# Kernel optimization log

Measured on AMD Instinct MI355X. Metric: run time of the kernel, lower is better.

Reference implementation:

```python
import jax, jax.numpy as jnp
import numpy as np

N = 100000      # nodes
E = 1600000     # edges
NINP = 64       # input node features
NE = 8          # edge attr channels (spectral supports)
NOUT = 24       # nout1 == nout2
NIN = 2 * NOUT  # 48, hidden width after concat
G = 256         # graphs in batch
EPS = 1e-5


def setup_inputs() -> dict:
    key = jax.random.key(0)
    ks = jax.random.split(key, 40)
    def nrm(i, shape, s=1.0):
        return jax.random.normal(ks[i], shape, dtype=jnp.float32) * s
    inp = {}
    inp["x"] = nrm(0, (N, NINP))
    inp["edge_index"] = jax.random.randint(ks[1], (2, E), 0, N)
    inp["edge_attr"] = nrm(2, (E, NE))
    inp["batch"] = jnp.sort(jax.random.randint(ks[3], (N,), 0, G))
    i = 4
    for l, din in ((1, NINP), (2, NIN), (3, NIN)):
        inp[f"W{l}"] = nrm(i, (NE, din, NOUT), 0.1); i += 1   # SpectConv weight [K,in,out]
        inp[f"b{l}"] = jnp.zeros((NOUT,), jnp.float32)         # SpectConv bias
        inp[f"A{l}"] = nrm(i, (din, NOUT), 0.1); i += 1        # fc11 weight
        inp[f"a{l}"] = jnp.zeros((NOUT,), jnp.float32)
        inp[f"B{l}"] = nrm(i, (din, NOUT), 0.1); i += 1        # fc12 weight
        inp[f"c{l}"] = jnp.zeros((NOUT,), jnp.float32)
        inp[f"g{l}"] = jnp.ones((NIN,), jnp.float32)           # BN gamma
        inp[f"be{l}"] = jnp.zeros((NIN,), jnp.float32)         # BN beta
    inp["F1"] = nrm(i, (NIN, 32), 0.1); i += 1
    inp["f1"] = jnp.zeros((32,), jnp.float32)
    inp["F2"] = nrm(i, (32, 1), 0.1); i += 1
    inp["f2"] = jnp.zeros((1,), jnp.float32)
    return inp


def _ml3(x, src, dst, ea, W, b, A, a, Bm, c):
    # SpectConv (selfconn=False): sum_k segment_sum(ea[:,k]*x[src] -> dst) @ W[k] + b
    xs = x[src]                                    # [E, F] gather
    acc = jnp.zeros((x.shape[0], W.shape[2]), x.dtype)
    for k in range(W.shape[0]):                    # small fixed K=NE loop
        h = jax.ops.segment_sum(ea[:, k:k+1] * xs, dst, num_segments=x.shape[0])
        acc = acc + h @ W[k]
    conv = jax.nn.relu(acc + b)
    gate = jax.nn.relu(x @ A + a) * jnp.tanh(x @ Bm + c)
    return jnp.concatenate([conv, gate], axis=1)   # [N, NIN]


def _bn(x, g, b):
    # BatchNorm1d, training mode (biased batch statistics)
    m = x.mean(0)
    v = x.var(0)
    return (x - m) * jax.lax.rsqrt(v + EPS) * g + b


def reference(x, edge_index, edge_attr, batch,
              W1, b1, A1, a1, B1, c1, g1, be1,
              W2, b2, A2, a2, B2, c2, g2, be2,
              W3, b3, A3, a3, B3, c3, g3, be3,
              F1, f1, F2, f2):
    src, dst = edge_index[0], edge_index[1]
    h = _bn(_ml3(x, src, dst, edge_attr, W1, b1, A1, a1, B1, c1), g1, be1)
    h = _bn(_ml3(h, src, dst, edge_attr, W2, b2, A2, a2, B2, c2), g2, be2)
    h = _bn(_ml3(h, src, dst, edge_attr, W3, b3, A3, a3, B3, c3), g3, be3)
    sums = jax.ops.segment_sum(h, batch, num_segments=G)
    cnts = jax.ops.segment_sum(jnp.ones((h.shape[0], 1), h.dtype), batch, num_segments=G)
    pooled = sums / jnp.maximum(cnts, 1.0)         # global_mean_pool
    return jax.nn.relu(pooled @ F1 + f1) @ F2 + f2  # [G, 1]
```

## Files before the change

### kernel.cpp

```cpp
#include <hip/hip_runtime.h>
#include <hip/hip_fp16.h>
#include <math.h>

#define N_NODES 100000
#define N_EDGES 1600000
#define NGRAPH  256
#define YCOLS   240
#define EPS     1e-5f
#define BNCHUNK 100

typedef _Float16 h2v __attribute__((ext_vector_type(2)));

#if defined(__has_builtin)
#if __has_builtin(__builtin_amdgcn_fdot2)
#define HAVE_FDOT2 1
#endif
#endif

__device__ inline float dot8(float4 yraw, float4 eraw, float acc) {
#ifdef HAVE_FDOT2
  union U { float4 f; h2v v[4]; } y, e;
  y.f = yraw; e.f = eraw;
  acc = __builtin_amdgcn_fdot2(y.v[0], e.v[0], acc, false);
  acc = __builtin_amdgcn_fdot2(y.v[1], e.v[1], acc, false);
  acc = __builtin_amdgcn_fdot2(y.v[2], e.v[2], acc, false);
  acc = __builtin_amdgcn_fdot2(y.v[3], e.v[3], acc, false);
#else
  const __half2* yh = reinterpret_cast<const __half2*>(&yraw);
  const __half2* eh = reinterpret_cast<const __half2*>(&eraw);
#pragma unroll
  for (int i = 0; i < 4; i++) {
    float2 a = __half22float2(yh[i]), b = __half22float2(eh[i]);
    acc += a.x * b.x + a.y * b.y;
  }
#endif
  return acc;
}

__global__ void k_count(const int* __restrict__ dst, int* __restrict__ deg) {
  int e = blockIdx.x * blockDim.x + threadIdx.x;
  if (e < N_EDGES) atomicAdd(&deg[dst[e]], 1);
}

__global__ void k_scan1(const int* __restrict__ deg, int* __restrict__ part,
                        int* __restrict__ bsum) {
  __shared__ int lds[256];
  int t = threadIdx.x;
  int base = blockIdx.x * 1024 + t * 4;
  int v[4]; int s = 0;
#pragma unroll
  for (int i = 0; i < 4; i++) { int idx = base + i; v[i] = (idx < N_NODES) ? deg[idx] : 0; s += v[i]; }
  lds[t] = s; __syncthreads();
  for (int off = 1; off < 256; off <<= 1) {
    int x = (t >= off) ? lds[t - off] : 0;
    __syncthreads();
    lds[t] += x;
    __syncthreads();
  }
  int excl = lds[t] - s;
#pragma unroll
  for (int i = 0; i < 4; i++) { int idx = base + i; if (idx < N_NODES) part[idx] = excl; excl += v[i]; }
  if (t == 255) bsum[blockIdx.x] = lds[255];
}

__global__ void k_scan2(int* __restrict__ bsum, int nb) {
  __shared__ int lds[128];
  int t = threadIdx.x;
  int v = (t < nb) ? bsum[t] : 0;
  lds[t] = v; __syncthreads();
  for (int off = 1; off < 128; off <<= 1) {
    int x = (t >= off) ? lds[t - off] : 0;
    __syncthreads();
    lds[t] += x;
    __syncthreads();
  }
  if (t < nb) bsum[t] = lds[t] - v;
}

__global__ void k_scan3(int* __restrict__ rowptr, const int* __restrict__ bsum,
                        int* __restrict__ cursor) {
  int i = blockIdx.x * blockDim.x + threadIdx.x;
  if (i < N_NODES) {
    int v = rowptr[i] + bsum[i >> 10];
    rowptr[i] = v; cursor[i] = v;
  }
  if (i == 0) rowptr[N_NODES] = N_EDGES;
}

__global__ void k_fill(const int* __restrict__ src, const int* __restrict__ dst,
                       const float* __restrict__ ea, int* __restrict__ cursor,
                       int* __restrict__ esrc, __half* __restrict__ ea_csr) {
  int e = blockIdx.x * blockDim.x + threadIdx.x;
  if (e < N_EDGES) {
    int d = dst[e];
    int pos = atomicAdd(&cursor[d], 1);
    esrc[pos] = src[e];
    float4 a = *reinterpret_cast<const float4*>(ea + (size_t)e * 8);
    float4 b = *reinterpret_cast<const float4*>(ea + (size_t)e * 8 + 4);
    union { __half h[8]; float4 f; } u;
    u.h[0] = __float2half(a.x); u.h[1] = __float2half(a.y);
    u.h[2] = __float2half(a.z); u.h[3] = __float2half(a.w);
    u.h[4] = __float2half(b.x); u.h[5] = __float2half(b.y);
    u.h[6] = __float2half(b.z); u.h[7] = __float2half(b.w);
    *reinterpret_cast<float4*>(ea_csr + (size_t)pos * 8) = u.f;
  }
}

__global__ void k_ghist(const int* __restrict__ batch, int* __restrict__ gcnt) {
  __shared__ int lh[NGRAPH];
  int t = threadIdx.x;
  lh[t] = 0; __syncthreads();
  for (int i = blockIdx.x * 256 + t; i < N_NODES; i += gridDim.x * 256)
    atomicAdd(&lh[batch[i]], 1);
  __syncthreads();
  if (lh[t]) atomicAdd(&gcnt[t], lh[t]);
}

__global__ void k_gscan(const int* __restrict__ gcnt, int* __restrict__ gstart) {
  __shared__ int lds[NGRAPH];
  int t = threadIdx.x;
  int v = gcnt[t]; lds[t] = v; __syncthreads();
  for (int off = 1; off < NGRAPH; off <<= 1) {
    int x = (t >= off) ? lds[t - off] : 0;
    __syncthreads();
    lds[t] += x;
    __syncthreads();
  }
  gstart[t] = lds[t] - v;
  if (t == NGRAPH - 1) gstart[NGRAPH] = lds[NGRAPH - 1];
}

__global__ void k_wcat(const float* __restrict__ W, const float* __restrict__ A,
                       const float* __restrict__ B, float* __restrict__ out, int din) {
  int i = blockIdx.x * blockDim.x + threadIdx.x;
  int total = din * YCOLS;
  if (i >= total) return;
  int f = i / YCOLS, j = i - f * YCOLS;
  float v;
  if (j < 192)      { int k = j / 24, o = j - k * 24; v = W[(k * din + f) * 24 + o]; }
  else if (j < 216) v = A[f * 24 + (j - 192)];
  else              v = B[f * 24 + (j - 216)];
  out[i] = v;
}

template <int F>
__global__ __launch_bounds__(256) void k_mm(const float* __restrict__ X,
                                            const float* __restrict__ Wc,
                                            const float* __restrict__ ss,
                                            __half* __restrict__ Yh,
                                            float* __restrict__ G) {
  __shared__ float sx[16 * F];
  int t = threadIdx.x;
  int r0 = blockIdx.x * 16;
  for (int i = t; i < 16 * F; i += 256) {
    int r = i / F, f = i - r * F;
    int row = r0 + r;
    float v = (row < N_NODES) ? X[(size_t)row * F + f] : 0.f;
    if (ss) v = v * ss[f] + ss[48 + f];
    sx[i] = v;
  }
  __syncthreads();
  if (t < YCOLS) {
    float acc[16];
#pragma unroll
    for (int r = 0; r < 16; r++) acc[r] = 0.f;
    for (int f = 0; f < F; f += 4) {
      float w0 = Wc[(f + 0) * YCOLS + t];
      float w1 = Wc[(f + 1) * YCOLS + t];
      float w2 = Wc[(f + 2) * YCOLS + t];
      float w3 = Wc[(f + 3) * YCOLS + t];
#pragma unroll
      for (int r = 0; r < 16; r++) {
        const float4 xv = *reinterpret_cast<const float4*>(&sx[r * F + f]);
        acc[r] += xv.x * w0 + xv.y * w1 + xv.z * w2 + xv.w * w3;
      }
    }
    int ycol = (t % 24) * 8 + t / 24;
    int gc   = (t < 216) ? (t - 192) : (24 + t - 216);
#pragma unroll
    for (int r = 0; r < 16; r++) {
      int row = r0 + r;
      if (row < N_NODES) {
        if (t < 192) Yh[(size_t)row * 192 + ycol] = __float2half(acc[r]);
        else         G[(size_t)row * 48 + gc] = acc[r];
      }
    }
  }
}

__global__ __launch_bounds__(192) void k_agg(
    const __half* __restrict__ Yh, const float* __restrict__ G,
    const int* __restrict__ rowptr, const int* __restrict__ esrc,
    const __half* __restrict__ ea_csr,
    const float* __restrict__ bconv, const float* __restrict__ ba,
    const float* __restrict__ bc,
    float* __restrict__ h, float* __restrict__ partial) {
  __shared__ float ssum[48], ssq[48];
  __shared__ float lacc[2][4][24];
  int t = threadIdx.x;
  if (t < 48) { ssum[t] = 0.f; ssq[t] = 0.f; }
  int ln   = t / 96;
  int slot = (t / 24) % 4;
  int o    = t % 24;
  int n = blockIdx.x * 2 + ln;
  float acc = 0.f;
  if (n < N_NODES) {
    int r0 = rowptr[n], r1 = rowptr[n + 1];
    int idx = r0 + slot;
    for (; idx + 4 < r1; idx += 8) {
      int s0 = esrc[idx], s1 = esrc[idx + 4];
      float4 e0 = *reinterpret_cast<const float4*>(ea_csr + (size_t)idx * 8);
      float4 e1 = *reinterpret_cast<const float4*>(ea_csr + (size_t)(idx + 4) * 8);
      float4 y0 = *reinterpret_cast<const float4*>(Yh + (size_t)s0 * 192 + o * 8);
      float4 y1 = *reinterpret_cast<const float4*>(Yh + (size_t)s1 * 192 + o * 8);
      acc = dot8(y0, e0, acc);
      acc = dot8(y1, e1, acc);
    }
    if (idx < r1) {
      int s0 = esrc[idx];
      float4 e0 = *reinterpret_cast<const float4*>(ea_csr + (size_t)idx * 8);
      float4 y0 = *reinterpret_cast<const float4*>(Yh + (size_t)s0 * 192 + o * 8);
      acc = dot8(y0, e0, acc);
    }
  }
  lacc[ln][slot][o] = acc;
  __syncthreads();
  if (t < 48) {
    int ln2 = t / 24, oo = t % 24;
    int n2 = blockIdx.x * 2 + ln2;
    if (n2 < N_NODES) {
      float a = lacc[ln2][0][oo] + lacc[ln2][1][oo] + lacc[ln2][2][oo] + lacc[ln2][3][oo];
      float conv = fmaxf(a + bconv[oo], 0.f);
      const float* gr = &G[(size_t)n2 * 48];
      float gate = fmaxf(gr[oo] + ba[oo], 0.f) * tanhf(gr[24 + oo] + bc[oo]);
      float* hr = &h[(size_t)n2 * 48];
      hr[oo] = conv;
      hr[24 + oo] = gate;
      atomicAdd(&ssum[oo], conv);        atomicAdd(&ssq[oo], conv * conv);
      atomicAdd(&ssum[24 + oo], gate);   atomicAdd(&ssq[24 + oo], gate * gate);
    }
  }
  __syncthreads();
  if (t < 96) partial[(size_t)blockIdx.x * 96 + t] = (t < 48) ? ssum[t] : ssq[t - 48];
}

__global__ __launch_bounds__(192) void k_bnred1(const float* __restrict__ partial,
                                                int nrows,
                                                float* __restrict__ out) {
  __shared__ float lds[192];
  int t = threadIdx.x;
  int rp = t / 96;
  int c  = t % 96;
  int r0 = blockIdx.x * BNCHUNK;
  int r1 = r0 + BNCHUNK; if (r1 > nrows) r1 = nrows;
  float s = 0.f;
  for (int r = r0 + rp; r < r1; r += 2) s += partial[(size_t)r * 96 + c];
  lds[t] = s; __syncthreads();
  if (t < 96) out[(size_t)blockIdx.x * 96 + t] = lds[t] + lds[t + 96];
}

__global__ void k_bnstats(const float* __restrict__ partial, int nblk,
                          const float* __restrict__ g, const float* __restrict__ be,
                          float* __restrict__ ss) {
  __shared__ float ls[256], lq[256];
  int c = blockIdx.x, t = threadIdx.x;
  float s = 0.f, q = 0.f;
  for (int i = t; i < nblk; i += 256) { s += partial[(size_t)i * 96 + c]; q += partial[(size_t)i * 96 + 48 + c]; }
  ls[t] = s; lq[t] = q; __syncthreads();
  for (int off = 128; off > 0; off >>= 1) {
    if (t < off) { ls[t] += ls[t + off]; lq[t] += lq[t + off]; }
    __syncthreads();
  }
  if (t == 0) {
    float mean = ls[0] / (float)N_NODES;
    float var = lq[0] / (float)N_NODES - mean * mean;
    var = fmaxf(var, 0.f);
    float sc = g[c] * rsqrtf(var + EPS);
    ss[c] = sc;
    ss[48 + c] = be[c] - mean * sc;
  }
}

__global__ __launch_bounds__(240) void k_pool2(const float* __restrict__ h,
                                               const int* __restrict__ gstart,
                                               const float* __restrict__ ss,
                                               float* __restrict__ pooled) {
  __shared__ float acc[240];
  int g = blockIdx.x, t = threadIdx.x;
  int o = t % 48, r = t / 48;
  int n0 = gstart[g], n1 = gstart[g + 1];
  float s = 0.f;
  for (int n = n0 + r; n < n1; n += 5) s += h[(size_t)n * 48 + o];
  acc[t] = s; __syncthreads();
  if (t < 48) {
    float tot = acc[t] + acc[t + 48] + acc[t + 96] + acc[t + 144] + acc[t + 192];
    float cnt = (float)(n1 - n0);
    float mean = tot / fmaxf(cnt, 1.f);
    pooled[g * 48 + t] = mean * ss[t] + ss[48 + t];
  }
}

__global__ __launch_bounds__(64) void k_mlp(const float* __restrict__ pooled,
                                            const float* __restrict__ F1,
                                            const float* __restrict__ f1,
                                            const float* __restrict__ F2,
                                            const float* __restrict__ f2,
                                            float* __restrict__ out) {
  __shared__ float p[48];
  int g = blockIdx.x, t = threadIdx.x;
  if (t < 48) p[t] = pooled[g * 48 + t];
  __syncthreads();
  float r = 0.f;
  if (t < 32) {
    float s = f1[t];
#pragma unroll
    for (int c = 0; c < 48; c++) s += p[c] * F1[c * 32 + t];
    r = fmaxf(s, 0.f) * F2[t];
  }
  for (int off = 32; off > 0; off >>= 1) r += __shfl_down(r, off, 64);
  if (t == 0) out[g] = r + f2[0];
}

extern "C" void kernel_launch(void* const* d_in, const int* in_sizes, int n_in,
                              void* d_out, int out_size, void* d_ws, size_t ws_size,
                              hipStream_t stream) {
  const float* x          = (const float*)d_in[0];
  const int*   edge_index = (const int*)d_in[1];
  const float* ea         = (const float*)d_in[2];
  const int*   batch      = (const int*)d_in[3];
  const float *W[3], *bcv[3], *A[3], *ba[3], *B[3], *bc[3], *g[3], *be[3];
  for (int l = 0; l < 3; l++) {
    int base = 4 + l * 8;
    W[l]   = (const float*)d_in[base + 0];
    bcv[l] = (const float*)d_in[base + 1];
    A[l]   = (const float*)d_in[base + 2];
    ba[l]  = (const float*)d_in[base + 3];
    B[l]   = (const float*)d_in[base + 4];
    bc[l]  = (const float*)d_in[base + 5];
    g[l]   = (const float*)d_in[base + 6];
    be[l]  = (const float*)d_in[base + 7];
  }
  const float* F1 = (const float*)d_in[28];
  const float* f1 = (const float*)d_in[29];
  const float* F2 = (const float*)d_in[30];
  const float* f2 = (const float*)d_in[31];
  const int* src = edge_index;
  const int* dst = edge_index + N_EDGES;

  char* w = (char*)d_ws;
  auto alloc = [&](size_t bytes) -> char* {
    char* p = w;
    w += (bytes + 255) & ~(size_t)255;
    return p;
  };
  int nagg = (N_NODES + 1) / 2;
  int nred = (nagg + BNCHUNK - 1) / BNCHUNK;

  int*    rowptr  = (int*)alloc((N_NODES + 1) * 4);
  int*    cursor  = (int*)alloc((size_t)N_NODES * 4);
  int*    deg     = (int*)alloc((size_t)N_NODES * 4);
  int*    bsum    = (int*)alloc(128 * 4);
  int*    esrc    = (int*)alloc((size_t)N_EDGES * 4);
  __half* ea_csr  = (__half*)alloc((size_t)N_EDGES * 8 * 2);
  int*    gcnt    = (int*)alloc(NGRAPH * 4);
  int*    gstart  = (int*)alloc((NGRAPH + 1) * 4);
  float*  Wc1     = (float*)alloc(64 * 240 * 4);
  float*  Wc2     = (float*)alloc(48 * 240 * 4);
  float*  Wc3     = (float*)alloc(48 * 240 * 4);
  __half* Yh      = (__half*)alloc((size_t)N_NODES * 192 * 2);
  float*  G       = (float*)alloc((size_t)N_NODES * 48 * 4);
  float*  h       = (float*)alloc((size_t)N_NODES * 48 * 4);
  float*  partial = (float*)alloc((size_t)nagg * 96 * 4);
  float*  partial2= (float*)alloc((size_t)nred * 96 * 4);
  float*  ss1     = (float*)alloc(96 * 4);
  float*  ss2     = (float*)alloc(96 * 4);
  float*  ss3     = (float*)alloc(96 * 4);
  float*  pooled  = (float*)alloc(NGRAPH * 48 * 4);

  hipMemsetAsync(deg, 0, (size_t)N_NODES * 4, stream);
  hipMemsetAsync(gcnt, 0, NGRAPH * 4, stream);

  k_count<<<(N_EDGES + 255) / 256, 256, 0, stream>>>(dst, deg);
  int nchunk = (N_NODES + 1023) / 1024;
  k_scan1<<<nchunk, 256, 0, stream>>>(deg, rowptr, bsum);
  k_scan2<<<1, 128, 0, stream>>>(bsum, nchunk);
  k_scan3<<<(N_NODES + 255) / 256, 256, 0, stream>>>(rowptr, bsum, cursor);
  k_fill<<<(N_EDGES + 255) / 256, 256, 0, stream>>>(src, dst, ea, cursor, esrc, ea_csr);

  k_ghist<<<64, 256, 0, stream>>>(batch, gcnt);
  k_gscan<<<1, NGRAPH, 0, stream>>>(gcnt, gstart);

  k_wcat<<<(64 * YCOLS + 255) / 256, 256, 0, stream>>>(W[0], A[0], B[0], Wc1, 64);
  k_wcat<<<(48 * YCOLS + 255) / 256, 256, 0, stream>>>(W[1], A[1], B[1], Wc2, 48);
  k_wcat<<<(48 * YCOLS + 255) / 256, 256, 0, stream>>>(W[2], A[2], B[2], Wc3, 48);

  int nmm  = (N_NODES + 15) / 16;

  k_mm<64><<<nmm, 256, 0, stream>>>(x, Wc1, nullptr, Yh, G);
  k_agg<<<nagg, 192, 0, stream>>>(Yh, G, rowptr, esrc, ea_csr, bcv[0], ba[0], bc[0], h, partial);
  k_bnred1<<<nred, 192, 0, stream>>>(partial, nagg, partial2);
  k_bnstats<<<48, 256, 0, stream>>>(partial2, nred, g[0], be[0], ss1);
  k_mm<48><<<nmm, 256, 0, stream>>>(h, Wc2, ss1, Yh, G);
  k_agg<<<nagg, 192, 0, stream>>>(Yh, G, rowptr, esrc, ea_csr, bcv[1], ba[1], bc[1], h, partial);
  k_bnred1<<<nred, 192, 0, stream>>>(partial, nagg, partial2);
  k_bnstats<<<48, 256, 0, stream>>>(partial2, nred, g[1], be[1], ss2);
  k_mm<48><<<nmm, 256, 0, stream>>>(h, Wc3, ss2, Yh, G);
  k_agg<<<nagg, 192, 0, stream>>>(Yh, G, rowptr, esrc, ea_csr, bcv[2], ba[2], bc[2], h, partial);
  k_bnred1<<<nred, 192, 0, stream>>>(partial, nagg, partial2);
  k_bnstats<<<48, 256, 0, stream>>>(partial2, nred, g[2], be[2], ss3);

  k_pool2<<<NGRAPH, 240, 0, stream>>>(h, gstart, ss3, pooled);
  k_mlp<<<NGRAPH, 64, 0, stream>>>(pooled, F1, f1, F2, f2, (float*)d_out);
}
```

Before: 762.4 us.

## Use fp16 MFMA for node projection GEMM with transposed half weights

Replaces the scalar-FMA per-layer node GEMM (X times concatenated weights, 240 columns) with MFMA 16x16x32 f16 instructions. Input rows are converted to fp16 in LDS, 64 rows per block, and K is padded to 64 with zeros for the 48-wide layers. The weights are prepacked as transposed fp16. This cuts ALU work in the GEMM but adds fp16 rounding of activations and weights, and the output stores are scattered per MFMA lane.

```diff
diff --git a/kernel.cpp b/kernel.cpp
--- a/kernel.cpp
+++ b/kernel.cpp
@@ -9,7 +9,9 @@
 #define EPS     1e-5f
 #define BNCHUNK 100
 
-typedef _Float16 h2v __attribute__((ext_vector_type(2)));
+typedef _Float16 h2v  __attribute__((ext_vector_type(2)));
+typedef _Float16 f16x8 __attribute__((ext_vector_type(8)));
+typedef float    f32x4 __attribute__((ext_vector_type(4)));
 
 #if defined(__has_builtin)
 #if __has_builtin(__builtin_amdgcn_fdot2)
@@ -130,59 +132,82 @@
   if (t == NGRAPH - 1) gstart[NGRAPH] = lds[NGRAPH - 1];
 }
 
-__global__ void k_wcat(const float* __restrict__ W, const float* __restrict__ A,
-                       const float* __restrict__ B, float* __restrict__ out, int din) {
+__global__ void k_wcat_h(const float* __restrict__ W, const float* __restrict__ A,
+                         const float* __restrict__ B, __half* __restrict__ out,
+                         int din) {
   int i = blockIdx.x * blockDim.x + threadIdx.x;
-  int total = din * YCOLS;
-  if (i >= total) return;
-  int f = i / YCOLS, j = i - f * YCOLS;
-  float v;
-  if (j < 192)      { int k = j / 24, o = j - k * 24; v = W[(k * din + f) * 24 + o]; }
-  else if (j < 216) v = A[f * 24 + (j - 192)];
-  else              v = B[f * 24 + (j - 216)];
-  out[i] = v;
+  if (i >= YCOLS * 64) return;
+  int j = i / 64, f = i % 64;
+  float v = 0.f;
+  if (f < din) {
+    if (j < 192)      { int k8 = j / 24, o = j - k8 * 24; v = W[(k8 * din + f) * 24 + o]; }
+    else if (j < 216) v = A[f * 24 + (j - 192)];
+    else              v = B[f * 24 + (j - 216)];
+  }
+  out[i] = __float2half(v);
 }
 
 template <int F>
 __global__ __launch_bounds__(256) void k_mm(const float* __restrict__ X,
-                                            const float* __restrict__ Wc,
+                                            const __half* __restrict__ Wct,
                                             const float* __restrict__ ss,
                                             __half* __restrict__ Yh,
                                             float* __restrict__ G) {
-  __shared__ float sx[16 * F];
-  int t = threadIdx.x;
-  int r0 = blockIdx.x * 16;
-  for (int i = t; i < 16 * F; i += 256) {
-    int r = i / F, f = i - r * F;
-    int row = r0 + r;
-    float v = (row < N_NODES) ? X[(size_t)row * F + f] : 0.f;
-    if (ss) v = v * ss[f] + ss[48 + f];
-    sx[i] = v;
+  __shared__ _Float16 sx[64][64];
+  int t = threadIdx.x;
+  int r0 = blockIdx.x * 64;
+  constexpr int F4 = F / 4;
+  for (int i = t; i < 64 * F4; i += 256) {
+    int row = i / F4, c4 = i - row * F4;
+    int grow = r0 + row;
+    float4 v = make_float4(0.f, 0.f, 0.f, 0.f);
+    if (grow < N_NODES) {
+      v = *reinterpret_cast<const float4*>(X + (size_t)grow * F + c4 * 4);
+      if (ss) {
+        int f = c4 * 4;
+        v.x = v.x * ss[f + 0] + ss[48 + f + 0];
+        v.y = v.y * ss[f + 1] + ss[48 + f + 1];
+        v.z = v.z * ss[f + 2] + ss[48 + f + 2];
+        v.w = v.w * ss[f + 3] + ss[48 + f + 3];
+      }
+    }
+    int c = c4 * 4;
+    sx[row][c + 0] = (_Float16)v.x;
+    sx[row][c + 1] = (_Float16)v.y;
+    sx[row][c + 2] = (_Float16)v.z;
+    sx[row][c + 3] = (_Float16)v.w;
+  }
+  if (F == 48) {
+    for (int i = t; i < 64 * 16; i += 256) {
+      int row = i / 16, k = 48 + (i - (i / 16) * 16);
+      sx[row][k] = (_Float16)0.f;
+    }
   }
   __syncthreads();
-  if (t < YCOLS) {
-    float acc[16];
-#pragma unroll
-    for (int r = 0; r < 16; r++) acc[r] = 0.f;
-    for (int f = 0; f < F; f += 4) {
-      float w0 = Wc[(f + 0) * YCOLS + t];
-      float w1 = Wc[(f + 1) * YCOLS + t];
-      float w2 = Wc[(f + 2) * YCOLS + t];
-      float w3 = Wc[(f + 3) * YCOLS + t];
-#pragma unroll
-      for (int r = 0; r < 16; r++) {
-        const float4 xv = *reinterpret_cast<const float4*>(&sx[r * F + f]);
-        acc[r] += xv.x * w0 + xv.y * w1 + xv.z * w2 + xv.w * w3;
-      }
-    }
-    int ycol = (t % 24) * 8 + t / 24;
-    int gc   = (t < 216) ? (t - 192) : (24 + t - 216);
-#pragma unroll
-    for (int r = 0; r < 16; r++) {
-      int row = r0 + r;
-      if (row < N_NODES) {
-        if (t < 192) Yh[(size_t)row * 192 + ycol] = __float2half(acc[r]);
-        else         G[(size_t)row * 48 + gc] = acc[r];
+
+  int w = t >> 6, l = t & 63;
+  int lrow = l & 15;
+  int lk = (l >> 4) * 8;
+  const f16x8 a0 = *reinterpret_cast<const f16x8*>(&sx[w * 16 + lrow][lk]);
+  const f16x8 a1 = *reinterpret_cast<const f16x8*>(&sx[w * 16 + lrow][lk + 32]);
+  const _Float16* wct = reinterpret_cast<const _Float16*>(Wct);
+
+#pragma unroll
+  for (int ct = 0; ct < 15; ct++) {
+    int col = ct * 16 + lrow;
+    f16x8 b0 = *reinterpret_cast<const f16x8*>(wct + col * 64 + lk);
+    f16x8 b1 = *reinterpret_cast<const f16x8*>(wct + col * 64 + lk + 32);
+    f32x4 acc = {0.f, 0.f, 0.f, 0.f};
+    acc = __builtin_amdgcn_mfma_f32_16x16x32_f16(a0, b0, acc, 0, 0, 0);
+    acc = __builtin_amdgcn_mfma_f32_16x16x32_f16(a1, b1, acc, 0, 0, 0);
+    int ycol = (col % 24) * 8 + col / 24;
+    int gc   = (col < 216) ? (col - 192) : (24 + col - 216);
+#pragma unroll
+    for (int r = 0; r < 4; r++) {
+      int grow = r0 + w * 16 + (l >> 4) * 4 + r;
+      if (grow < N_NODES) {
+        if (col < 192) Yh[(size_t)grow * 192 + ycol] = __float2half(acc[r]);
+        else           G[(size_t)grow * 48 + gc] = acc[r];
       }
     }
   }
@@ -364,9 +389,9 @@
   __half* ea_csr  = (__half*)alloc((size_t)N_EDGES * 8 * 2);
   int*    gcnt    = (int*)alloc(NGRAPH * 4);
   int*    gstart  = (int*)alloc((NGRAPH + 1) * 4);
-  float*  Wc1     = (float*)alloc(64 * 240 * 4);
-  float*  Wc2     = (float*)alloc(48 * 240 * 4);
-  float*  Wc3     = (float*)alloc(48 * 240 * 4);
+  __half* Wct1    = (__half*)alloc((size_t)YCOLS * 64 * 2);
+  __half* Wct2    = (__half*)alloc((size_t)YCOLS * 64 * 2);
+  __half* Wct3    = (__half*)alloc((size_t)YCOLS * 64 * 2);
   __half* Yh      = (__half*)alloc((size_t)N_NODES * 192 * 2);
   float*  G       = (float*)alloc((size_t)N_NODES * 48 * 4);
   float*  h       = (float*)alloc((size_t)N_NODES * 48 * 4);
@@ -390,21 +415,21 @@
   k_ghist<<<64, 256, 0, stream>>>(batch, gcnt);
   k_gscan<<<1, NGRAPH, 0, stream>>>(gcnt, gstart);
 
-  k_wcat<<<(64 * YCOLS + 255) / 256, 256, 0, stream>>>(W[0], A[0], B[0], Wc1, 64);
-  k_wcat<<<(48 * YCOLS + 255) / 256, 256, 0, stream>>>(W[1], A[1], B[1], Wc2, 48);
-  k_wcat<<<(48 * YCOLS + 255) / 256, 256, 0, stream>>>(W[2], A[2], B[2], Wc3, 48);
-
-  int nmm  = (N_NODES + 15) / 16;
-
-  k_mm<64><<<nmm, 256, 0, stream>>>(x, Wc1, nullptr, Yh, G);
+  k_wcat_h<<<(YCOLS * 64 + 255) / 256, 256, 0, stream>>>(W[0], A[0], B[0], Wct1, 64);
+  k_wcat_h<<<(YCOLS * 64 + 255) / 256, 256, 0, stream>>>(W[1], A[1], B[1], Wct2, 48);
+  k_wcat_h<<<(YCOLS * 64 + 255) / 256, 256, 0, stream>>>(W[2], A[2], B[2], Wct3, 48);
+
+  int nmm = (N_NODES + 63) / 64;
+
+  k_mm<64><<<nmm, 256, 0, stream>>>(x, Wct1, nullptr, Yh, G);
   k_agg<<<nagg, 192, 0, stream>>>(Yh, G, rowptr, esrc, ea_csr, bcv[0], ba[0], bc[0], h, partial);
   k_bnred1<<<nred, 192, 0, stream>>>(partial, nagg, partial2);
   k_bnstats<<<48, 256, 0, stream>>>(partial2, nred, g[0], be[0], ss1);
-  k_mm<48><<<nmm, 256, 0, stream>>>(h, Wc2, ss1, Yh, G);
+  k_mm<48><<<nmm, 256, 0, stream>>>(h, Wct2, ss1, Yh, G);
   k_agg<<<nagg, 192, 0, stream>>>(Yh, G, rowptr, esrc, ea_csr, bcv[1], ba[1], bc[1], h, partial);
   k_bnred1<<<nred, 192, 0, stream>>>(partial, nagg, partial2);
   k_bnstats<<<48, 256, 0, stream>>>(partial2, nred, g[1], be[1], ss2);
-  k_mm<48><<<nmm, 256, 0, stream>>>(h, Wc3, ss2, Yh, G);
+  k_mm<48><<<nmm, 256, 0, stream>>>(h, Wct3, ss2, Yh, G);
   k_agg<<<nagg, 192, 0, stream>>>(Yh, G, rowptr, esrc, ea_csr, bcv[2], ba[2], bc[2], h, partial);
   k_bnred1<<<nred, 192, 0, stream>>>(partial, nagg, partial2);
   k_bnstats<<<48, 256, 0, stream>>>(partial2, nred, g[2], be[2], ss3);
```

Result: faster. 707.7 us (-7.2%).
